# Kernel tuning notes

Hardware: AMD Instinct MI355X
Metric: run time of the kernel (lower is better)

## Reference

```python
import jax, jax.numpy as jnp
import numpy as np

NOISE_DIM = 128
IN_FEATURES = 512
OUT_FEATURES = 512
BATCH = 256


def setup_inputs() -> dict:
    key = jax.random.key(0)
    k1, k2, k3 = jax.random.split(key, 3)
    out_dim = IN_FEATURES * OUT_FEATURES + OUT_FEATURES
    # x = [noise | features]
    x = jax.random.normal(k1, (BATCH, NOISE_DIM + IN_FEATURES), dtype=jnp.float32)
    # hypermodel Linear params; scale ~ 1/sqrt(fan_in) like torch default init
    scale = 1.0 / np.sqrt(NOISE_DIM)
    W = jax.random.uniform(k2, (NOISE_DIM, out_dim), dtype=jnp.float32, minval=-scale, maxval=scale)
    b = jax.random.uniform(k3, (out_dim,), dtype=jnp.float32, minval=-scale, maxval=scale)
    return {"x": x, "W": W, "b": b}


def reference(x, W, b):
    # split input into hypernet noise and features
    noise = x[:, :NOISE_DIM]            # [B, noise_dim]
    feats = x[:, NOISE_DIM:]            # [B, in_features]
    # hypermodel: generate per-sample linear params
    params = noise @ W + b              # [B, in*out + out]
    w_flat = params[:, : IN_FEATURES * OUT_FEATURES]
    bias = params[:, IN_FEATURES * OUT_FEATURES :]        # [B, out]
    weight = w_flat.reshape(-1, IN_FEATURES, OUT_FEATURES)  # [B, in, out]
    # batched matmul (torch.bmm of [B,1,in] @ [B,in,out]) + bias, squeeze
    out = jnp.einsum("bi,bio->bo", feats, weight) + bias   # [B, out]
    return out
```

## Files before the change

### kernel.cpp

```cpp
#include <hip/hip_runtime.h>
#include <hip/hip_bf16.h>
#include <stdint.h>

namespace {
constexpr int kBatch = 256;
constexpr int kNoise = 128;
constexpr int kIn    = 512;
constexpr int kOut   = 512;
constexpr int kXCols = kNoise + kIn;
constexpr int kPCols = kIn * kOut + kOut;
constexpr int kOTile = 32;
constexpr int kITile = 16;
constexpr int kSplits = kIn / kITile;
constexpr int kWStride = 68;
constexpr int kFeatsStride = 260;
constexpr int kSlab = kBatch * kOut + 64;
}

typedef __bf16 bf16x8 __attribute__((ext_vector_type(8)));
typedef float  f32x4  __attribute__((ext_vector_type(4)));
typedef unsigned int u32x4 __attribute__((ext_vector_type(4)));

__device__ inline unsigned int pack_bf16x2(float lo, float hi) {
    unsigned int a = (unsigned int)__builtin_bit_cast(unsigned short, (__bf16)lo);
    unsigned int b = (unsigned int)__builtin_bit_cast(unsigned short, (__bf16)hi);
    return a | (b << 16);
}

__device__ inline void wg_barrier_lds() {
    __asm__ volatile("" ::: "memory");
    __builtin_amdgcn_s_waitcnt(0xC07F);
    __builtin_amdgcn_s_barrier();
    __asm__ volatile("" ::: "memory");
}

__global__ __launch_bounds__(512, 4)
void hyper_gemm_kernel(const float* __restrict__ x,
                       const float* __restrict__ W,
                       const float* __restrict__ bvec,
                       float* __restrict__ part)
{
    const int tid  = threadIdx.x;
    const int lane = tid & 63;
    const int wave = tid >> 6;
    const int q    = lane >> 4;
    const int l16  = lane & 15;

    const int o0 = blockIdx.x * kOTile;
    const int i0 = blockIdx.y * kITile;

    const int sw = tid >> 5;
    const int sc = tid & 31;

    __shared__ unsigned int wtile[2][kOTile * kWStride];
    __shared__ float feats_lds[kITile * kFeatsStride];
    __shared__ float bv_lds[(kITile + 1) * kOTile];

    const int nPass = (blockIdx.y == 0) ? (kITile + 1) : kITile;

    auto pass_cbase = [&](int p) -> size_t {
        return (p == kITile) ? (size_t)(kIn * kOut) : (size_t)(i0 + p) * kOut;
    };
    const float* wbase = W + (size_t)(8 * sw) * kPCols + o0 + sc;
    auto loadpass = [&](int p, float* r) {
        const float* wp = wbase + pass_cbase(p);
        #pragma unroll
        for (int rr = 0; rr < 8; ++rr) r[rr] = wp[(size_t)rr * kPCols];
    };

    float r0[8], rA[8], rB[8], rC[8];
    loadpass(0, r0);
    loadpass(1, rA);
    loadpass(2, rB);
    loadpass(3, rC);

    for (int idx = tid; idx < (kITile + 1) * kOTile; idx += 512) {
        const int p = idx >> 5, c = idx & 31;
        const size_t cb = (p == kITile) ? (size_t)(kIn * kOut) : (size_t)(i0 + p) * kOut;
        bv_lds[idx] = bvec[cb + o0 + c];
    }

    {
        const int i    = tid & 15;
        const int brow = tid >> 4;
        #pragma unroll
        for (int rep = 0; rep < 8; ++rep) {
            const int b = brow + rep * 32;
            feats_lds[i * kFeatsStride + b] = x[b * kXCols + kNoise + i0 + i];
        }
    }

    bf16x8 afrag[2][4];
    #pragma unroll
    for (int rt = 0; rt < 2; ++rt) {
        const float* xr = x + (size_t)(wave * 32 + rt * 16 + l16) * kXCols;
        #pragma unroll
        for (int s = 0; s < 4; ++s) {
            const float* p = xr + s * 32 + q * 8;
            f32x4 u0 = *(const f32x4*)(p);
            f32x4 u1 = *(const f32x4*)(p + 4);
            bf16x8 a;
            a[0] = (__bf16)u0[0]; a[1] = (__bf16)u0[1];
            a[2] = (__bf16)u0[2]; a[3] = (__bf16)u0[3];
            a[4] = (__bf16)u1[0]; a[5] = (__bf16)u1[1];
            a[6] = (__bf16)u1[2]; a[7] = (__bf16)u1[3];
            afrag[rt][s] = a;
        }
    }

    {
        u32x4 pk;
        #pragma unroll
        for (int j = 0; j < 4; ++j) pk[j] = pack_bf16x2(r0[2 * j], r0[2 * j + 1]);
        *(u32x4*)&wtile[0][sc * kWStride + 4 * sw] = pk;
    }

    float oacc[2][2][4];
    #pragma unroll
    for (int rt = 0; rt < 2; ++rt)
        #pragma unroll
        for (int nt = 0; nt < 2; ++nt)
            #pragma unroll
            for (int r = 0; r < 4; ++r) oacc[rt][nt][r] = 0.f;

    for (int ip = 0; ip < nPass; ++ip) {
        wg_barrier_lds();

        if (ip + 1 < nPass) {
            u32x4 pk;
            #pragma unroll
            for (int j = 0; j < 4; ++j) pk[j] = pack_bf16x2(rA[2 * j], rA[2 * j + 1]);
            *(u32x4*)&wtile[(ip + 1) & 1][sc * kWStride + 4 * sw] = pk;
        }
        #pragma unroll
        for (int rr = 0; rr < 8; ++rr) { rA[rr] = rB[rr]; rB[rr] = rC[rr]; }
        if (ip + 4 < nPass) loadpass(ip + 4, rC);

        const unsigned int* wt = &wtile[ip & 1][0];
        f32x4 acc[2][2];
        const f32x4 zero = {0.f, 0.f, 0.f, 0.f};
        acc[0][0] = zero; acc[0][1] = zero; acc[1][0] = zero; acc[1][1] = zero;

        #pragma unroll
        for (int s = 0; s < 4; ++s) {
            #pragma unroll
            for (int nt = 0; nt < 2; ++nt) {
                u32x4 raw = *(const u32x4*)&wt[(nt * 16 + l16) * kWStride + s * 16 + q * 4];
                bf16x8 bfrag = __builtin_bit_cast(bf16x8, raw);
                acc[0][nt] = __builtin_amdgcn_mfma_f32_16x16x32_bf16(
                    afrag[0][s], bfrag, acc[0][nt], 0, 0, 0);
                acc[1][nt] = __builtin_amdgcn_mfma_f32_16x16x32_bf16(
                    afrag[1][s], bfrag, acc[1][nt], 0, 0, 0);
            }
        }

        const float bv0 = bv_lds[ip * kOTile + l16];
        const float bv1 = bv_lds[ip * kOTile + 16 + l16];

        if (ip < kITile) {
            #pragma unroll
            for (int rt = 0; rt < 2; ++rt) {
                const f32x4 f4 = *(const f32x4*)&feats_lds[ip * kFeatsStride
                                        + wave * 32 + rt * 16 + q * 4];
                #pragma unroll
                for (int r = 0; r < 4; ++r) {
                    oacc[rt][0][r] += f4[r] * (acc[rt][0][r] + bv0);
                    oacc[rt][1][r] += f4[r] * (acc[rt][1][r] + bv1);
                }
            }
        } else {
            #pragma unroll
            for (int rt = 0; rt < 2; ++rt)
                #pragma unroll
                for (int r = 0; r < 4; ++r) {
                    oacc[rt][0][r] += acc[rt][0][r] + bv0;
                    oacc[rt][1][r] += acc[rt][1][r] + bv1;
                }
        }
    }

    float* pp = part + (size_t)blockIdx.y * kSlab;
    #pragma unroll
    for (int rt = 0; rt < 2; ++rt)
        #pragma unroll
        for (int nt = 0; nt < 2; ++nt) {
            const int o = o0 + nt * 16 + l16;
            #pragma unroll
            for (int r = 0; r < 4; ++r) {
                const int b = wave * 32 + rt * 16 + q * 4 + r;
                pp[(size_t)b * kOut + o] = oacc[rt][nt][r];
            }
        }
}

__global__ __launch_bounds__(128)
void reduce_kernel(const float* __restrict__ part, float* __restrict__ out)
{
    const size_t idx4 = ((size_t)blockIdx.x * 128 + threadIdx.x) * 4;
    f32x4 a0 = {0.f, 0.f, 0.f, 0.f};
    f32x4 a1 = {0.f, 0.f, 0.f, 0.f};
    #pragma unroll
    for (int s = 0; s < kSplits; s += 2) {
        a0 += *(const f32x4*)(part + (size_t)s * kSlab + idx4);
        a1 += *(const f32x4*)(part + (size_t)(s + 1) * kSlab + idx4);
    }
    *(f32x4*)(out + idx4) = a0 + a1;
}

extern "C" void kernel_launch(void* const* d_in, const int* in_sizes, int n_in,
                              void* d_out, int out_size, void* d_ws, size_t ws_size,
                              hipStream_t stream) {
    const float* x  = (const float*)d_in[0];
    const float* W  = (const float*)d_in[1];
    const float* bv = (const float*)d_in[2];
    float* out  = (float*)d_out;
    float* part = (float*)d_ws;

    dim3 grid(kOut / kOTile, kSplits);
    hyper_gemm_kernel<<<grid, 512, 0, stream>>>(x, W, bv, part);

    const int n4 = kBatch * kOut / 4;
    reduce_kernel<<<n4 / 128, 128, 0, stream>>>(part, out);
}
```

Baseline: 213.7 us.

## Widen output tile to 64 columns with 1024-thread blocks, 16 rows per wave

Doubles the output-column tile to 64 and the block size to 1024 threads. Each of the 16 waves now covers 16 batch rows and 4 column sub-tiles, where before 8 waves each covered 32 rows and 2 sub-tiles. This halves the grid along the output dimension and gives each loaded weight tile more reuse per block. The cost is a larger LDS footprint, fewer blocks to spread across the chip, and a launch bound that may limit occupancy or register allocation.

```diff
diff --git a/kernel.cpp b/kernel.cpp
--- a/kernel.cpp
+++ b/kernel.cpp
@@ -9,7 +9,7 @@
 constexpr int kOut   = 512;
 constexpr int kXCols = kNoise + kIn;
 constexpr int kPCols = kIn * kOut + kOut;
-constexpr int kOTile = 32;
+constexpr int kOTile = 64;
 constexpr int kITile = 16;
 constexpr int kSplits = kIn / kITile;
 constexpr int kWStride = 68;
@@ -34,7 +34,7 @@
     __asm__ volatile("" ::: "memory");
 }
 
-__global__ __launch_bounds__(512, 4)
+__global__ __launch_bounds__(1024, 4)
 void hyper_gemm_kernel(const float* __restrict__ x,
                        const float* __restrict__ W,
                        const float* __restrict__ bvec,
@@ -49,8 +49,8 @@
     const int o0 = blockIdx.x * kOTile;
     const int i0 = blockIdx.y * kITile;
 
-    const int sw = tid >> 5;
-    const int sc = tid & 31;
+    const int sw = tid >> 6;
+    const int sc = tid & 63;
 
     __shared__ unsigned int wtile[2][kOTile * kWStride];
     __shared__ float feats_lds[kITile * kFeatsStride];
@@ -74,8 +74,8 @@
     loadpass(2, rB);
     loadpass(3, rC);
 
-    for (int idx = tid; idx < (kITile + 1) * kOTile; idx += 512) {
-        const int p = idx >> 5, c = idx & 31;
+    for (int idx = tid; idx < (kITile + 1) * kOTile; idx += 1024) {
+        const int p = idx >> 6, c = idx & 63;
         const size_t cb = (p == kITile) ? (size_t)(kIn * kOut) : (size_t)(i0 + p) * kOut;
         bv_lds[idx] = bvec[cb + o0 + c];
     }
@@ -84,16 +84,15 @@
         const int i    = tid & 15;
         const int brow = tid >> 4;
         #pragma unroll
-        for (int rep = 0; rep < 8; ++rep) {
-            const int b = brow + rep * 32;
+        for (int rep = 0; rep < 4; ++rep) {
+            const int b = brow + rep * 64;
             feats_lds[i * kFeatsStride + b] = x[b * kXCols + kNoise + i0 + i];
         }
     }
 
-    bf16x8 afrag[2][4];
-    #pragma unroll
-    for (int rt = 0; rt < 2; ++rt) {
-        const float* xr = x + (size_t)(wave * 32 + rt * 16 + l16) * kXCols;
+    bf16x8 afrag[4];
+    {
+        const float* xr = x + (size_t)(wave * 16 + l16) * kXCols;
         #pragma unroll
         for (int s = 0; s < 4; ++s) {
             const float* p = xr + s * 32 + q * 8;
@@ -104,7 +103,7 @@
             a[2] = (__bf16)u0[2]; a[3] = (__bf16)u0[3];
             a[4] = (__bf16)u1[0]; a[5] = (__bf16)u1[1];
             a[6] = (__bf16)u1[2]; a[7] = (__bf16)u1[3];
-            afrag[rt][s] = a;
+            afrag[s] = a;
         }
     }
 
@@ -115,13 +114,11 @@
         *(u32x4*)&wtile[0][sc * kWStride + 4 * sw] = pk;
     }
 
-    float oacc[2][2][4];
+    float oacc[4][4];
     #pragma unroll
-    for (int rt = 0; rt < 2; ++rt)
-        #pragma unroll
-        for (int nt = 0; nt < 2; ++nt)
-            #pragma unroll
-            for (int r = 0; r < 4; ++r) oacc[rt][nt][r] = 0.f;
+    for (int nt = 0; nt < 4; ++nt)
+        #pragma unroll
+        for (int r = 0; r < 4; ++r) oacc[nt][r] = 0.f;
 
     for (int ip = 0; ip < nPass; ++ip) {
         wg_barrier_lds();
@@ -137,60 +134,53 @@
         if (ip + 4 < nPass) loadpass(ip + 4, rC);
 
         const unsigned int* wt = &wtile[ip & 1][0];
-        f32x4 acc[2][2];
+        f32x4 acc[4];
         const f32x4 zero = {0.f, 0.f, 0.f, 0.f};
-        acc[0][0] = zero; acc[0][1] = zero; acc[1][0] = zero; acc[1][1] = zero;
+        #pragma unroll
+        for (int nt = 0; nt < 4; ++nt) acc[nt] = zero;
 
         #pragma unroll
         for (int s = 0; s < 4; ++s) {
             #pragma unroll
-            for (int nt = 0; nt < 2; ++nt) {
+            for (int nt = 0; nt < 4; ++nt) {
                 u32x4 raw = *(const u32x4*)&wt[(nt * 16 + l16) * kWStride + s * 16 + q * 4];
                 bf16x8 bfrag = __builtin_bit_cast(bf16x8, raw);
-                acc[0][nt] = __builtin_amdgcn_mfma_f32_16x16x32_bf16(
-                    afrag[0][s], bfrag, acc[0][nt], 0, 0, 0);
-                acc[1][nt] = __builtin_amdgcn_mfma_f32_16x16x32_bf16(
-                    afrag[1][s], bfrag, acc[1][nt], 0, 0, 0);
+                acc[nt] = __builtin_amdgcn_mfma_f32_16x16x32_bf16(
+                    afrag[s], bfrag, acc[nt], 0, 0, 0);
             }
         }
 
-        const float bv0 = bv_lds[ip * kOTile + l16];
-        const float bv1 = bv_lds[ip * kOTile + 16 + l16];
+        float bvv[4];
+        #pragma unroll
+        for (int nt = 0; nt < 4; ++nt) bvv[nt] = bv_lds[ip * kOTile + nt * 16 + l16];
 
         if (ip < kITile) {
-            #pragma unroll
-            for (int rt = 0; rt < 2; ++rt) {
-                const f32x4 f4 = *(const f32x4*)&feats_lds[ip * kFeatsStride
-                                        + wave * 32 + rt * 16 + q * 4];
+            const f32x4 f4 = *(const f32x4*)&feats_lds[ip * kFeatsStride
+                                    + wave * 16 + q * 4];
+            #pragma unroll
+            for (int nt = 0; nt < 4; ++nt)
                 #pragma unroll
-                for (int r = 0; r < 4; ++r) {
-                    oacc[rt][0][r] += f4[r] * (acc[rt][0][r] + bv0);
-                    oacc[rt][1][r] += f4[r] * (acc[rt][1][r] + bv1);
-                }
-            }
+                for (int r = 0; r < 4; ++r)
+                    oacc[nt][r] += f4[r] * (acc[nt][r] + bvv[nt]);
         } else {
             #pragma unroll
-            for (int rt = 0; rt < 2; ++rt)
+            for (int nt = 0; nt < 4; ++nt)
                 #pragma unroll
-                for (int r = 0; r < 4; ++r) {
-                    oacc[rt][0][r] += acc[rt][0][r] + bv0;
-                    oacc[rt][1][r] += acc[rt][1][r] + bv1;
-                }
+                for (int r = 0; r < 4; ++r)
+                    oacc[nt][r] += acc[nt][r] + bvv[nt];
         }
     }
 
     float* pp = part + (size_t)blockIdx.y * kSlab;
     #pragma unroll
-    for (int rt = 0; rt < 2; ++rt)
-        #pragma unroll
-        for (int nt = 0; nt < 2; ++nt) {
-            const int o = o0 + nt * 16 + l16;
-            #pragma unroll
-            for (int r = 0; r < 4; ++r) {
-                const int b = wave * 32 + rt * 16 + q * 4 + r;
-                pp[(size_t)b * kOut + o] = oacc[rt][nt][r];
-            }
-        }
+    for (int nt = 0; nt < 4; ++nt) {
+        const int o = o0 + nt * 16 + l16;
+        #pragma unroll
+        for (int r = 0; r < 4; ++r) {
+            const int b = wave * 16 + q * 4 + r;
+            pp[(size_t)b * kOut + o] = oacc[nt][r];
+        }
+    }
 }
 
 __global__ __launch_bounds__(128)
@@ -217,7 +207,7 @@
     float* part = (float*)d_ws;
 
     dim3 grid(kOut / kOTile, kSplits);
-    hyper_gemm_kernel<<<grid, 512, 0, stream>>>(x, W, bv, part);
+    hyper_gemm_kernel<<<grid, 1024, 0, stream>>>(x, W, bv, part);
 
     const int n4 = kBatch * kOut / 4;
     reduce_kernel<<<n4 / 128, 128, 0, stream>>>(part, out);
```

New measurement: 215.2 us. No clear change (+0.7%).
